# Kernel tuning notes

Hardware: AMD Instinct MI355X
Metric: run time of the kernel (lower is better)

Reference implementation:

```python
import jax, jax.numpy as jnp
import numpy as np
from jax import lax

B, T, C = 4, 1024, 1024
NH, HD = 16, 64
SCALE = 1.0 / np.sqrt(HD)
LN_EPS = 1e-5


def _layernorm(x, g, b):
    mu = jnp.mean(x, axis=-1, keepdims=True)
    var = jnp.var(x, axis=-1, keepdims=True)
    return (x - mu) * lax.rsqrt(var + LN_EPS) * g + b


def _compress(seg, w, g, b):
    # seg: [B, nH, L, hd]; depthwise Conv1d(k=2, s=2, p=1, groups=hd, no bias) + LayerNorm(hd)
    Bs, nH, L, hd = seg.shape
    xc = seg.reshape(Bs * nH, L, hd).transpose(0, 2, 1)  # [B*nH, hd, L]
    y = lax.conv_general_dilated(xc, w, window_strides=(2,), padding=[(1, 1)],
                                 dimension_numbers=('NCH', 'OIH', 'NCH'),
                                 feature_group_count=hd)  # [B*nH, hd, L//2+1]
    y = y.transpose(0, 2, 1)
    y = _layernorm(y, g, b)
    return y.reshape(Bs, nH, -1, hd)


def setup_inputs() -> dict:
    key = jax.random.key(0)
    ks = jax.random.split(key, 16)
    d = {
        'x': jax.random.normal(ks[0], (B, T, C), jnp.float32),
        'mem_k1': jax.random.normal(ks[1], (B, NH, 129, HD), jnp.float32),
        'mem_v1': jax.random.normal(ks[2], (B, NH, 129, HD), jnp.float32),
        'mem_k2': jax.random.normal(ks[3], (B, NH, 257, HD), jnp.float32),
        'mem_v2': jax.random.normal(ks[4], (B, NH, 257, HD), jnp.float32),
        'mem_k3': jax.random.normal(ks[5], (B, NH, 513, HD), jnp.float32),
        'mem_v3': jax.random.normal(ks[6], (B, NH, 513, HD), jnp.float32),
        'c_attn_w': jax.random.normal(ks[7], (3 * C, C), jnp.float32) * 0.02,
        'c_attn_b': jnp.zeros((3 * C,), jnp.float32),
        'c_proj_w': jax.random.normal(ks[8], (C, C), jnp.float32) * 0.02,
        'c_proj_b': jnp.zeros((C,), jnp.float32),
        'compress_k_w': jax.random.normal(ks[9], (HD, 1, 2), jnp.float32) * 0.5,
        'ln_k_g': jnp.ones((HD,), jnp.float32),
        'ln_k_b': jnp.zeros((HD,), jnp.float32),
        'compress_v_w': jax.random.normal(ks[10], (HD, 1, 2), jnp.float32) * 0.5,
        'ln_v_g': jnp.ones((HD,), jnp.float32),
        'ln_v_b': jnp.zeros((HD,), jnp.float32),
    }
    return d


def reference(x, mem_k1, mem_v1, mem_k2, mem_v2, mem_k3, mem_v3,
              c_attn_w, c_attn_b, c_proj_w, c_proj_b,
              compress_k_w, ln_k_g, ln_k_b, compress_v_w, ln_v_g, ln_v_b):
    # qkv projection
    qkv = x @ c_attn_w.T + c_attn_b  # [B, T, 3C]
    q, k_new, v_new = jnp.split(qkv, 3, axis=2)
    q = q.reshape(B, T, NH, HD).transpose(0, 2, 1, 3)       # [B, nH, T, hd]
    k_new = k_new.reshape(B, T, NH, HD).transpose(0, 2, 1, 3)
    v_new = v_new.reshape(B, T, NH, HD).transpose(0, 2, 1, 3)

    # compress the most recent cached segment (513 -> 257)
    k3c = _compress(mem_k3, compress_k_w, ln_k_g, ln_k_b)
    v3c = _compress(mem_v3, compress_v_w, ln_v_g, ln_v_b)

    all_k = jnp.concatenate([mem_k1, mem_k2, k3c, k_new], axis=2)  # [B, nH, T_mem, hd]
    all_v = jnp.concatenate([mem_v1, mem_v2, v3c, v_new], axis=2)
    T_mem = all_k.shape[2]

    att = jnp.einsum('bhqd,bhkd->bhqk', q, all_k) * SCALE  # [B, nH, T, T_mem]
    # causal mask taken from tril(block_size)[:T, :T_mem]: row i attends cols j <= i
    mask = jnp.arange(T)[:, None] >= jnp.arange(T_mem)[None, :]
    att = jnp.where(mask, att, -jnp.inf)
    att = jax.nn.softmax(att, axis=-1)
    y = jnp.einsum('bhqk,bhkd->bhqd', att, all_v)  # [B, nH, T, hd]
    y = y.transpose(0, 2, 1, 3).reshape(B, T, C)
    y = y @ c_proj_w.T + c_proj_b
    return y
```

## Files before the change

kernel.cpp:

```cpp
#include <hip/hip_runtime.h>


using u16    = unsigned short;
using bf16x8 = __attribute__((ext_vector_type(8))) __bf16;
using f32x4  = __attribute__((ext_vector_type(4))) float;
using u16x8  = __attribute__((ext_vector_type(8))) unsigned short;
using u16x4  = __attribute__((ext_vector_type(4))) unsigned short;

__device__ __forceinline__ u16 f2bf(float f) {
    union { float f; unsigned u; } v; v.f = f;
    unsigned r = v.u + 0x7FFFu + ((v.u >> 16) & 1u);
    return (u16)(r >> 16);
}

__device__ __forceinline__ void gload16(const void* src, const void* lds_base) {
    __builtin_amdgcn_global_load_lds(
        (const __attribute__((address_space(1))) void*)src,
        (__attribute__((address_space(3))) void*)lds_base, 16, 0, 0);
}

__global__ void cvt_f32_bf16(const float* __restrict__ src, u16* __restrict__ dst, int n4) {
    int i = blockIdx.x * blockDim.x + threadIdx.x;
    if (i >= n4) return;
    float4 f = reinterpret_cast<const float4*>(src)[i];
    u16x4 o; o[0] = f2bf(f.x); o[1] = f2bf(f.y); o[2] = f2bf(f.z); o[3] = f2bf(f.w);
    reinterpret_cast<u16x4*>(dst)[i] = o;
}

__global__ __launch_bounds__(64) void copy_mem_rows(const float* __restrict__ src,
                                                    u16* __restrict__ dst, int L, int ro) {
    int bh = blockIdx.y, t = blockIdx.x, d = threadIdx.x;
    float v = src[((size_t)bh * L + t) * 64 + d];
    dst[((size_t)bh * 1024 + ro + t) * 64 + d] = f2bf(v);
}

__global__ __launch_bounds__(64) void compress_ln(const float* __restrict__ src,
                                                  const float* __restrict__ w,
                                                  const float* __restrict__ g,
                                                  const float* __restrict__ bta,
                                                  u16* __restrict__ dst, int ro) {
    int bh = blockIdx.y, t = blockIdx.x, d = threadIdx.x;
    const float* seg = src + (size_t)bh * 513 * 64;
    float x0 = (t > 0) ? seg[(size_t)(2 * t - 1) * 64 + d] : 0.f;
    float x1 = seg[(size_t)(2 * t) * 64 + d];
    float y = w[2 * d] * x0 + w[2 * d + 1] * x1;
    float s = y;
    #pragma unroll
    for (int o = 32; o; o >>= 1) s += __shfl_xor(s, o);
    float mu = s * (1.f / 64.f);
    float dv = y - mu;
    float s2 = dv * dv;
    #pragma unroll
    for (int o = 32; o; o >>= 1) s2 += __shfl_xor(s2, o);
    float var = s2 * (1.f / 64.f);
    float out = dv * rsqrtf(var + 1e-5f) * g[d] + bta[d];
    dst[((size_t)bh * 1024 + ro + t) * 64 + d] = f2bf(out);
}

__global__ __launch_bounds__(256) void transpose_v(const u16* __restrict__ src,
                                                   u16* __restrict__ dst) {
    __shared__ u16 tile[64][66];
    const int bh = blockIdx.y, t0 = blockIdx.x * 64;
    const int tid = threadIdx.x;
    #pragma unroll
    for (int i = 0; i < 2; ++i) {
        int p = tid + i * 256;
        int tr = p >> 3, dc = (p & 7) * 8;
        *(u16x8*)&tile[tr][dc] = *(const u16x8*)&src[((size_t)bh * 1024 + t0 + tr) * 64 + dc];
    }
    __syncthreads();
    #pragma unroll
    for (int i = 0; i < 2; ++i) {
        int p = tid + i * 256;
        int d = p >> 3, tc = (p & 7) * 8;
        u16x8 v;
        #pragma unroll
        for (int e = 0; e < 8; ++e) v[e] = tile[tc + e][d];
        *(u16x8*)&dst[((size_t)bh * 64 + d) * 1024 + t0 + tc] = v;
    }
}

__global__ __launch_bounds__(256) void gemm128(const u16* __restrict__ A,
                                               const u16* __restrict__ Bw,
                                               const float* __restrict__ bias,
                                               int K, int N, int mode,
                                               float* __restrict__ outF,
                                               u16* __restrict__ q_buf,
                                               u16* __restrict__ all_k,
                                               u16* __restrict__ all_v) {
    __shared__ __align__(16) u16 Al[128 * 64];
    __shared__ __align__(16) u16 Bl[128 * 64];
    const int tid = threadIdx.x;
    const int wv = tid >> 6, lane = tid & 63;
    const int lg = lane >> 4, lr = lane & 15;
    const int wr = (wv >> 1) * 64, wc = (wv & 1) * 64;
    const int m0 = blockIdx.x * 128, n0 = blockIdx.y * 128;
    f32x4 acc[4][4] = {};
    const int ob0 = wv * 4096;
    for (int kt = 0; kt < K; kt += 64) {
        __syncthreads();
        #pragma unroll
        for (int c = 0; c < 4; ++c) {
            int ob = ob0 + c * 1024;
            int o = ob + lane * 16;
            int r = o >> 7, cb = o & 127;
            gload16((const char*)A + (((size_t)(m0 + r) * K + kt) << 1) + cb, (char*)Al + ob);
            gload16((const char*)Bw + (((size_t)(n0 + r) * K + kt) << 1) + cb, (char*)Bl + ob);
        }
        __syncthreads();
        #pragma unroll
        for (int dh = 0; dh < 2; ++dh) {
            bf16x8 af[4], bq[4];
            #pragma unroll
            for (int mi = 0; mi < 4; ++mi)
                af[mi] = *(const bf16x8*)&Al[(wr + mi * 16 + lr) * 64 + dh * 32 + lg * 8];
            #pragma unroll
            for (int ni = 0; ni < 4; ++ni)
                bq[ni] = *(const bf16x8*)&Bl[(wc + ni * 16 + lr) * 64 + dh * 32 + lg * 8];
            __builtin_amdgcn_s_setprio(1);
            #pragma unroll
            for (int mi = 0; mi < 4; ++mi)
                #pragma unroll
                for (int ni = 0; ni < 4; ++ni)
                    acc[mi][ni] = __builtin_amdgcn_mfma_f32_16x16x32_bf16(af[mi], bq[ni], acc[mi][ni], 0, 0, 0);
            __builtin_amdgcn_s_setprio(0);
        }
    }
    #pragma unroll
    for (int mi = 0; mi < 4; ++mi)
        #pragma unroll
        for (int ni = 0; ni < 4; ++ni)
            #pragma unroll
            for (int r = 0; r < 4; ++r) {
                int mm = m0 + wr + mi * 16 + lg * 4 + r;
                int nn = n0 + wc + ni * 16 + lr;
                float v = acc[mi][ni][r] + bias[nn];
                if (mode == 0) {
                    outF[(size_t)mm * N + nn] = v;
                } else {
                    int which = nn >> 10, c = nn & 1023, h = c >> 6, d = c & 63;
                    int b = mm >> 10, t = mm & 1023;
                    int bh = b * 16 + h;
                    if (which == 0) {
                        q_buf[((size_t)bh * 1024 + t) * 64 + d] = f2bf(v * 0.125f);
                    } else if (t < 381) {
                        u16* dst = (which == 1) ? all_k : all_v;
                        dst[((size_t)bh * 1024 + 643 + t) * 64 + d] = f2bf(v);
                    }
                }
            }
}

__global__ __launch_bounds__(256) void attn_kernel(const u16* __restrict__ Q,
                                                   const u16* __restrict__ Kc,
                                                   const u16* __restrict__ VT,
                                                   u16* __restrict__ Y) {
    __shared__ __align__(16) u16 Kl[2][4096];
    __shared__ __align__(16) u16 Vl[2][4096];
    __shared__ __align__(16) u16 P_w[4][16 * 64];
    const int tid = threadIdx.x;
    const int lane = tid & 63;
    const int w = tid >> 6;
    const int lg = lane >> 4, lr = lane & 15;
    const int bh = blockIdx.x;
    const int pair = blockIdx.y;
    const u16* Kb = Kc + (size_t)bh * 65536;
    const u16* Vb = VT + (size_t)bh * 65536;
    char* Pbase = (char*)&P_w[w][0];
    const int xorq = (lr & 7) << 4;

    const int r0 = tid >> 3,         c0 = ((tid & 7) * 16) ^ ((r0 & 7) << 4);
    const int r1 = (tid + 256) >> 3, c1 = ((tid & 7) * 16) ^ ((r1 & 7) << 4);
    const int dst0 = w * 1024;

    for (int phase = 0; phase < 2; ++phase) {
        const int qt = phase ? (15 - pair) : pair;
        const int q0 = qt * 64;
        const u16* Qb = Q + ((size_t)bh * 1024 + q0 + w * 16) * 64;
        bf16x8 qf0 = *(const bf16x8*)&Qb[lr * 64 + lg * 8];
        bf16x8 qf1 = *(const bf16x8*)&Qb[lr * 64 + 32 + lg * 8];
        f32x4 o[4] = {};
        float m = -1e30f, lsum = 0.f;
        const int i_q = q0 + w * 16 + lr;

        {
            const char* Ks = (const char*)Kb;
            gload16(Ks + ((size_t)r0 << 7) + c0, (char*)&Kl[0][0] + dst0);
            gload16(Ks + ((size_t)r1 << 7) + c1, (char*)&Kl[0][0] + 4096 + dst0);
            gload16((const char*)Vb + ((size_t)r0 << 11) + c0, (char*)&Vl[0][0] + dst0);
            gload16((const char*)Vb + ((size_t)r1 << 11) + c1, (char*)&Vl[0][0] + 4096 + dst0);
        }
        __syncthreads();
        int cur = 0;

        for (int kt = 0; kt <= qt; ++kt) {
            if (kt < qt) {
                const int k0n = (kt + 1) * 64;
                const char* Ks = (const char*)Kb + ((size_t)k0n << 7);
                const char* Vs = (const char*)Vb + ((size_t)k0n << 1);
                char* Kd = (char*)&Kl[cur ^ 1][0];
                char* Vd = (char*)&Vl[cur ^ 1][0];
                gload16(Ks + ((size_t)r0 << 7) + c0, Kd + dst0);
                gload16(Ks + ((size_t)r1 << 7) + c1, Kd + 4096 + dst0);
                gload16(Vs + ((size_t)r0 << 11) + c0, Vd + dst0);
                gload16(Vs + ((size_t)r1 << 11) + c1, Vd + 4096 + dst0);
            }
            const char* Kt = (const char*)&Kl[cur][0];
            const char* Vt = (const char*)&Vl[cur][0];
            f32x4 st[4] = {};
            __builtin_amdgcn_s_setprio(1);
            #pragma unroll
            for (int hh = 0; hh < 4; ++hh) {
                const char* Kr = Kt + (size_t)(hh * 16 + lr) * 128;
                bf16x8 kf0 = *(const bf16x8*)(Kr + ((lg * 16) ^ xorq));
                bf16x8 kf1 = *(const bf16x8*)(Kr + ((64 + lg * 16) ^ xorq));
                st[hh] = __builtin_amdgcn_mfma_f32_16x16x32_bf16(kf0, qf0, st[hh], 0, 0, 0);
                st[hh] = __builtin_amdgcn_mfma_f32_16x16x32_bf16(kf1, qf1, st[hh], 0, 0, 0);
            }
            __builtin_amdgcn_s_setprio(0);
            const int k0 = kt * 64;
            float sv[16];
            float tmax = -1e30f;
            if (kt == qt) {
                #pragma unroll
                for (int hh = 0; hh < 4; ++hh)
                    #pragma unroll
                    for (int r = 0; r < 4; ++r) {
                        int j = k0 + hh * 16 + lg * 4 + r;
                        float s = (j <= i_q) ? st[hh][r] : -1e30f;
                        sv[hh * 4 + r] = s;
                        tmax = fmaxf(tmax, s);
                    }
            } else {
                #pragma unroll
                for (int hh = 0; hh < 4; ++hh)
                    #pragma unroll
                    for (int r = 0; r < 4; ++r) {
                        float s = st[hh][r];
                        sv[hh * 4 + r] = s;
                        tmax = fmaxf(tmax, s);
                    }
            }
            tmax = fmaxf(tmax, __shfl_xor(tmax, 16));
            tmax = fmaxf(tmax, __shfl_xor(tmax, 32));
            if (!__all(tmax - m <= 8.f)) {
                float mnew = fmaxf(m, tmax);
                float alpha = __expf(m - mnew);
                #pragma unroll
                for (int c = 0; c < 4; ++c) {
                    o[c][0] *= alpha; o[c][1] *= alpha; o[c][2] *= alpha; o[c][3] *= alpha;
                }
                lsum *= alpha;
                m = mnew;
            }
            float psum = 0.f;
            #pragma unroll
            for (int hh = 0; hh < 4; ++hh) {
                u16x4 pk;
                #pragma unroll
                for (int r = 0; r < 4; ++r) {
                    float p = __expf(sv[hh * 4 + r] - m);
                    psum += p;
                    pk[r] = f2bf(p);
                }
                *(u16x4*)(Pbase + lr * 128 + ((hh * 32 + lg * 8) ^ xorq)) = pk;
            }
            psum += __shfl_xor(psum, 16);
            psum += __shfl_xor(psum, 32);
            lsum += psum;
            asm volatile("s_waitcnt lgkmcnt(0)" ::: "memory");
            __builtin_amdgcn_sched_barrier(0);
            #pragma unroll
            for (int ks = 0; ks < 2; ++ks) {
                bf16x8 pf = *(const bf16x8*)(Pbase + lr * 128 + ((ks * 64 + lg * 16) ^ xorq));
                __builtin_amdgcn_s_setprio(1);
                #pragma unroll
                for (int c = 0; c < 4; ++c) {
                    const char* Vr = Vt + (size_t)(c * 16 + lr) * 128;
                    bf16x8 vf = *(const bf16x8*)(Vr + ((ks * 64 + lg * 16) ^ xorq));
                    o[c] = __builtin_amdgcn_mfma_f32_16x16x32_bf16(vf, pf, o[c], 0, 0, 0);
                }
                __builtin_amdgcn_s_setprio(0);
            }
            __syncthreads();
            cur ^= 1;
        }
        float inv = 1.0f / lsum;
        #pragma unroll
        for (int c = 0; c < 4; ++c) {
            u16x4 ov;
            #pragma unroll
            for (int r = 0; r < 4; ++r) ov[r] = f2bf(o[c][r] * inv);
            *(u16x4*)(Pbase + lr * 128 + (((c * 16 + lg * 4) * 2) ^ xorq)) = ov;
        }
        asm volatile("s_waitcnt lgkmcnt(0)" ::: "memory");
        __builtin_amdgcn_sched_barrier(0);
        const int b = bh >> 4, h = bh & 15;
        const int qr = lane >> 2, dseg = (lane & 3) * 16;
        const int xorr = (qr & 7) << 4;
        size_t g = ((size_t)(b * 1024 + q0 + w * 16 + qr)) * 1024 + h * 64 + dseg;
        *(u16x8*)&Y[g]     = *(const u16x8*)(Pbase + qr * 128 + ((dseg * 2) ^ xorr));
        *(u16x8*)&Y[g + 8] = *(const u16x8*)(Pbase + qr * 128 + ((dseg * 2 + 16) ^ xorr));
    }
}

extern "C" void kernel_launch(void* const* d_in, const int* in_sizes, int n_in,
                              void* d_out, int out_size, void* d_ws, size_t ws_size,
                              hipStream_t stream) {
    const float* x            = (const float*)d_in[0];
    const float* mem_k1       = (const float*)d_in[1];
    const float* mem_v1       = (const float*)d_in[2];
    const float* mem_k2       = (const float*)d_in[3];
    const float* mem_v2       = (const float*)d_in[4];
    const float* mem_k3       = (const float*)d_in[5];
    const float* mem_v3       = (const float*)d_in[6];
    const float* c_attn_w     = (const float*)d_in[7];
    const float* c_attn_b     = (const float*)d_in[8];
    const float* c_proj_w     = (const float*)d_in[9];
    const float* c_proj_b     = (const float*)d_in[10];
    const float* compress_k_w = (const float*)d_in[11];
    const float* ln_k_g       = (const float*)d_in[12];
    const float* ln_k_b       = (const float*)d_in[13];
    const float* compress_v_w = (const float*)d_in[14];
    const float* ln_v_g       = (const float*)d_in[15];
    const float* ln_v_b       = (const float*)d_in[16];

    char* ws = (char*)d_ws;
    u16* x_bf   = (u16*)(ws);
    u16* all_vT = (u16*)(ws);
    u16* wq_bf  = (u16*)(ws + (8u << 20));
    u16* wp_bf  = (u16*)(ws + (14u << 20));
    u16* q_buf  = (u16*)(ws + (16u << 20));
    u16* all_k  = (u16*)(ws + (24u << 20));
    u16* all_v  = (u16*)(ws + (32u << 20));
    u16* att_y  = (u16*)(ws + (40u << 20));
    float* out = (float*)d_out;

    cvt_f32_bf16<<<4096, 256, 0, stream>>>(x, x_bf, 1048576);
    cvt_f32_bf16<<<3072, 256, 0, stream>>>(c_attn_w, wq_bf, 786432);
    cvt_f32_bf16<<<1024, 256, 0, stream>>>(c_proj_w, wp_bf, 262144);

    copy_mem_rows<<<dim3(129, 64), 64, 0, stream>>>(mem_k1, all_k, 129, 0);
    copy_mem_rows<<<dim3(129, 64), 64, 0, stream>>>(mem_v1, all_v, 129, 0);
    copy_mem_rows<<<dim3(257, 64), 64, 0, stream>>>(mem_k2, all_k, 257, 129);
    copy_mem_rows<<<dim3(257, 64), 64, 0, stream>>>(mem_v2, all_v, 257, 129);

    compress_ln<<<dim3(257, 64), 64, 0, stream>>>(mem_k3, compress_k_w, ln_k_g, ln_k_b, all_k, 386);
    compress_ln<<<dim3(257, 64), 64, 0, stream>>>(mem_v3, compress_v_w, ln_v_g, ln_v_b, all_v, 386);

    gemm128<<<dim3(32, 24), 256, 0, stream>>>(x_bf, wq_bf, c_attn_b, 1024, 3072, 1,
                                              nullptr, q_buf, all_k, all_v);

    transpose_v<<<dim3(16, 64), 256, 0, stream>>>(all_v, all_vT);

    attn_kernel<<<dim3(64, 8), 256, 0, stream>>>(q_buf, all_k, all_vT, att_y);

    gemm128<<<dim3(32, 8), 256, 0, stream>>>(att_y, wp_bf, c_proj_b, 1024, 1024, 0,
                                             out, nullptr, nullptr, nullptr);
}
```

Before: 140.4 us.

## Double-buffer GEMM LDS tiles and XOR-swizzle to avoid bank conflicts

Converts the bf16 GEMM main loop to a double-buffered LDS scheme that issues the next K-tile's global-to-LDS loads before computing on the current tile, with one barrier per iteration. It also applies an XOR swizzle on the column offset of each loaded row so fragment reads from LDS spread across banks. This doubles LDS usage to 64KB per block, which may lower occupancy, and relies on the barrier waiting for the async LDS loads.

```diff
diff --git a/kernel.cpp b/kernel.cpp
--- a/kernel.cpp
+++ b/kernel.cpp
@@ -88,8 +88,8 @@
                                                u16* __restrict__ q_buf,
                                                u16* __restrict__ all_k,
                                                u16* __restrict__ all_v) {
-    __shared__ __align__(16) u16 Al[128 * 64];
-    __shared__ __align__(16) u16 Bl[128 * 64];
+    __shared__ __align__(16) u16 Al[2][128 * 64];
+    __shared__ __align__(16) u16 Bl[2][128 * 64];
     const int tid = threadIdx.x;
     const int wv = tid >> 6, lane = tid & 63;
     const int lg = lane >> 4, lr = lane & 15;
@@ -97,26 +97,50 @@
     const int m0 = blockIdx.x * 128, n0 = blockIdx.y * 128;
     f32x4 acc[4][4] = {};
     const int ob0 = wv * 4096;
-    for (int kt = 0; kt < K; kt += 64) {
-        __syncthreads();
-        #pragma unroll
-        for (int c = 0; c < 4; ++c) {
-            int ob = ob0 + c * 1024;
-            int o = ob + lane * 16;
-            int r = o >> 7, cb = o & 127;
-            gload16((const char*)A + (((size_t)(m0 + r) * K + kt) << 1) + cb, (char*)Al + ob);
-            gload16((const char*)Bw + (((size_t)(n0 + r) * K + kt) << 1) + cb, (char*)Bl + ob);
-        }
-        __syncthreads();
+    int srow[4], scol[4];
+    #pragma unroll
+    for (int c = 0; c < 4; ++c) {
+        int o = ob0 + c * 1024 + lane * 16;
+        int r = o >> 7;
+        srow[c] = r;
+        scol[c] = (o & 127) ^ ((r & 7) << 4);
+    }
+    const int nk = K >> 6;
+    #pragma unroll
+    for (int c = 0; c < 4; ++c) {
+        int ob = ob0 + c * 1024;
+        gload16((const char*)A  + (((size_t)(m0 + srow[c]) * K) << 1) + scol[c], (char*)&Al[0][0] + ob);
+        gload16((const char*)Bw + (((size_t)(n0 + srow[c]) * K) << 1) + scol[c], (char*)&Bl[0][0] + ob);
+    }
+    __syncthreads();
+    int cur = 0;
+    for (int kt = 0; kt < nk; ++kt) {
+        if (kt + 1 < nk) {
+            const size_t ko = (size_t)(kt + 1) << 6;
+            #pragma unroll
+            for (int c = 0; c < 4; ++c) {
+                int ob = ob0 + c * 1024;
+                gload16((const char*)A  + (((size_t)(m0 + srow[c]) * K + ko) << 1) + scol[c],
+                        (char*)&Al[cur ^ 1][0] + ob);
+                gload16((const char*)Bw + (((size_t)(n0 + srow[c]) * K + ko) << 1) + scol[c],
+                        (char*)&Bl[cur ^ 1][0] + ob);
+            }
+        }
+        const char* At = (const char*)&Al[cur][0];
+        const char* Bt = (const char*)&Bl[cur][0];
         #pragma unroll
         for (int dh = 0; dh < 2; ++dh) {
             bf16x8 af[4], bq[4];
             #pragma unroll
-            for (int mi = 0; mi < 4; ++mi)
-                af[mi] = *(const bf16x8*)&Al[(wr + mi * 16 + lr) * 64 + dh * 32 + lg * 8];
-            #pragma unroll
-            for (int ni = 0; ni < 4; ++ni)
-                bq[ni] = *(const bf16x8*)&Bl[(wc + ni * 16 + lr) * 64 + dh * 32 + lg * 8];
+            for (int mi = 0; mi < 4; ++mi) {
+                int row = wr + mi * 16 + lr;
+                af[mi] = *(const bf16x8*)(At + row * 128 + ((dh * 64 + lg * 16) ^ ((row & 7) << 4)));
+            }
+            #pragma unroll
+            for (int ni = 0; ni < 4; ++ni) {
+                int row = wc + ni * 16 + lr;
+                bq[ni] = *(const bf16x8*)(Bt + row * 128 + ((dh * 64 + lg * 16) ^ ((row & 7) << 4)));
+            }
             __builtin_amdgcn_s_setprio(1);
             #pragma unroll
             for (int mi = 0; mi < 4; ++mi)
@@ -125,6 +149,8 @@
                     acc[mi][ni] = __builtin_amdgcn_mfma_f32_16x16x32_bf16(af[mi], bq[ni], acc[mi][ni], 0, 0, 0);
             __builtin_amdgcn_s_setprio(0);
         }
+        __syncthreads();
+        cur ^= 1;
     }
     #pragma unroll
     for (int mi = 0; mi < 4; ++mi)
```

Measured after the change: 145.8 us. 3.9% more time.

## Double-buffer GEMM LDS tiles with XOR swizzle and XCD-aware block remap

Applied to the files above, without the earlier changes.

Restructures the bf16 GEMM main loop to use two 128x32 LDS buffers per operand, issuing the next K-slice's global-to-LDS loads before the current slice's MFMAs so memory latency overlaps compute. It also applies an XOR swizzle to the LDS column layout to reduce bank conflicts, and remaps block IDs so consecutive tiles spread across the 8 XCDs. The K step halves to 32, which doubles the number of barriers and loop iterations. The remap assumes the grid size is divisible by 8.

```diff
diff --git a/kernel.cpp b/kernel.cpp
--- a/kernel.cpp
+++ b/kernel.cpp
@@ -88,43 +88,60 @@
                                                u16* __restrict__ q_buf,
                                                u16* __restrict__ all_k,
                                                u16* __restrict__ all_v) {
-    __shared__ __align__(16) u16 Al[128 * 64];
-    __shared__ __align__(16) u16 Bl[128 * 64];
+    __shared__ __align__(16) u16 Al[2][128 * 32];
+    __shared__ __align__(16) u16 Bl[2][128 * 32];
     const int tid = threadIdx.x;
     const int wv = tid >> 6, lane = tid & 63;
     const int lg = lane >> 4, lr = lane & 15;
     const int wr = (wv >> 1) * 64, wc = (wv & 1) * 64;
-    const int m0 = blockIdx.x * 128, n0 = blockIdx.y * 128;
+    const int id = blockIdx.x + blockIdx.y * gridDim.x;
+    const int per = (gridDim.x * gridDim.y) >> 3;
+    const int nid = (id & 7) * per + (id >> 3);
+    const int m0 = (nid % gridDim.x) * 128, n0 = (nid / gridDim.x) * 128;
     f32x4 acc[4][4] = {};
-    const int ob0 = wv * 4096;
-    for (int kt = 0; kt < K; kt += 64) {
+    const int sr0 = tid >> 2,         sc0 = (((tid & 3) << 4)) ^ (((sr0 >> 1) & 3) << 4);
+    const int sr1 = (tid + 256) >> 2, sc1 = (((tid & 3) << 4)) ^ (((sr1 >> 1) & 3) << 4);
+    const int dA0 = wv * 1024;
+    const int dA1 = 4096 + wv * 1024;
+    const int nk = K >> 5;
+    gload16((const char*)A  + (((size_t)(m0 + sr0) * K) << 1) + sc0, (char*)&Al[0][0] + dA0);
+    gload16((const char*)A  + (((size_t)(m0 + sr1) * K) << 1) + sc1, (char*)&Al[0][0] + dA1);
+    gload16((const char*)Bw + (((size_t)(n0 + sr0) * K) << 1) + sc0, (char*)&Bl[0][0] + dA0);
+    gload16((const char*)Bw + (((size_t)(n0 + sr1) * K) << 1) + sc1, (char*)&Bl[0][0] + dA1);
+    __syncthreads();
+    int cur = 0;
+    for (int kt = 0; kt < nk; ++kt) {
+        const char* At = (const char*)&Al[cur][0];
+        const char* Bt = (const char*)&Bl[cur][0];
+        bf16x8 af[4], bq[4];
+        #pragma unroll
+        for (int mi = 0; mi < 4; ++mi) {
+            int row = wr + mi * 16 + lr;
+            af[mi] = *(const bf16x8*)(At + row * 64 + ((lg << 4) ^ (((row >> 1) & 3) << 4)));
+        }
+        #pragma unroll
+        for (int ni = 0; ni < 4; ++ni) {
+            int row = wc + ni * 16 + lr;
+            bq[ni] = *(const bf16x8*)(Bt + row * 64 + ((lg << 4) ^ (((row >> 1) & 3) << 4)));
+        }
+        if (kt + 1 < nk) {
+            const size_t ko = (size_t)(kt + 1) << 5;
+            char* Ad = (char*)&Al[cur ^ 1][0];
+            char* Bd = (char*)&Bl[cur ^ 1][0];
+            gload16((const char*)A  + (((size_t)(m0 + sr0) * K + ko) << 1) + sc0, Ad + dA0);
+            gload16((const char*)A  + (((size_t)(m0 + sr1) * K + ko) << 1) + sc1, Ad + dA1);
+            gload16((const char*)Bw + (((size_t)(n0 + sr0) * K + ko) << 1) + sc0, Bd + dA0);
+            gload16((const char*)Bw + (((size_t)(n0 + sr1) * K + ko) << 1) + sc1, Bd + dA1);
+        }
+        __builtin_amdgcn_s_setprio(1);
+        #pragma unroll
+        for (int mi = 0; mi < 4; ++mi)
+            #pragma unroll
+            for (int ni = 0; ni < 4; ++ni)
+                acc[mi][ni] = __builtin_amdgcn_mfma_f32_16x16x32_bf16(af[mi], bq[ni], acc[mi][ni], 0, 0, 0);
+        __builtin_amdgcn_s_setprio(0);
         __syncthreads();
-        #pragma unroll
-        for (int c = 0; c < 4; ++c) {
-            int ob = ob0 + c * 1024;
-            int o = ob + lane * 16;
-            int r = o >> 7, cb = o & 127;
-            gload16((const char*)A + (((size_t)(m0 + r) * K + kt) << 1) + cb, (char*)Al + ob);
-            gload16((const char*)Bw + (((size_t)(n0 + r) * K + kt) << 1) + cb, (char*)Bl + ob);
-        }
-        __syncthreads();
-        #pragma unroll
-        for (int dh = 0; dh < 2; ++dh) {
-            bf16x8 af[4], bq[4];
-            #pragma unroll
-            for (int mi = 0; mi < 4; ++mi)
-                af[mi] = *(const bf16x8*)&Al[(wr + mi * 16 + lr) * 64 + dh * 32 + lg * 8];
-            #pragma unroll
-            for (int ni = 0; ni < 4; ++ni)
-                bq[ni] = *(const bf16x8*)&Bl[(wc + ni * 16 + lr) * 64 + dh * 32 + lg * 8];
-            __builtin_amdgcn_s_setprio(1);
-            #pragma unroll
-            for (int mi = 0; mi < 4; ++mi)
-                #pragma unroll
-                for (int ni = 0; ni < 4; ++ni)
-                    acc[mi][ni] = __builtin_amdgcn_mfma_f32_16x16x32_bf16(af[mi], bq[ni], acc[mi][ni], 0, 0, 0);
-            __builtin_amdgcn_s_setprio(0);
-        }
+        cur ^= 1;
     }
     #pragma unroll
     for (int mi = 0; mi < 4; ++mi)
```

Result: faster. 133.0 us (-5.3%).

## Replace 128x128 GEMM with 256x256 triple-buffered swizzled pipelined GEMM

Applied to the files above, without the earlier changes.

Swaps the 128x128 bf16 MFMA GEMM for a 256x256-tile kernel with 512 threads. It triple-buffers LDS, loading 32-wide K slices through global_load_lds, and overlaps the next stages' loads with MFMA work using explicit waitcnt, barriers and scheduling hints. It also adds an XOR swizzle on LDS rows to avoid bank conflicts and an XCD-aware block-to-tile remap for L2 locality. The larger tiles raise data reuse per block but cut the grid to 192 and 64 blocks, which may leave many CUs idle on both projections.

```diff
diff --git a/kernel.cpp b/kernel.cpp
--- a/kernel.cpp
+++ b/kernel.cpp
@@ -80,54 +80,102 @@
     }
 }
 
-__global__ __launch_bounds__(256) void gemm128(const u16* __restrict__ A,
-                                               const u16* __restrict__ Bw,
-                                               const float* __restrict__ bias,
-                                               int K, int N, int mode,
-                                               float* __restrict__ outF,
-                                               u16* __restrict__ q_buf,
-                                               u16* __restrict__ all_k,
-                                               u16* __restrict__ all_v) {
-    __shared__ __align__(16) u16 Al[128 * 64];
-    __shared__ __align__(16) u16 Bl[128 * 64];
-    const int tid = threadIdx.x;
-    const int wv = tid >> 6, lane = tid & 63;
+__global__ __launch_bounds__(512, 2) void gemm256p(const u16* __restrict__ A,
+                                                   const u16* __restrict__ Bw,
+                                                   const float* __restrict__ bias,
+                                                   int K, int N, int mode,
+                                                   float* __restrict__ outF,
+                                                   u16* __restrict__ q_buf,
+                                                   u16* __restrict__ all_k,
+                                                   u16* __restrict__ all_v) {
+    __shared__ __align__(16) u16 S[3][4][4096];
+    const int t = threadIdx.x;
+    const int wv = t >> 6, lane = t & 63;
     const int lg = lane >> 4, lr = lane & 15;
-    const int wr = (wv >> 1) * 64, wc = (wv & 1) * 64;
-    const int m0 = blockIdx.x * 128, n0 = blockIdx.y * 128;
-    f32x4 acc[4][4] = {};
-    const int ob0 = wv * 4096;
-    for (int kt = 0; kt < K; kt += 64) {
-        __syncthreads();
-        #pragma unroll
-        for (int c = 0; c < 4; ++c) {
-            int ob = ob0 + c * 1024;
-            int o = ob + lane * 16;
-            int r = o >> 7, cb = o & 127;
-            gload16((const char*)A + (((size_t)(m0 + r) * K + kt) << 1) + cb, (char*)Al + ob);
-            gload16((const char*)Bw + (((size_t)(n0 + r) * K + kt) << 1) + cb, (char*)Bl + ob);
-        }
-        __syncthreads();
-        #pragma unroll
-        for (int dh = 0; dh < 2; ++dh) {
-            bf16x8 af[4], bq[4];
-            #pragma unroll
-            for (int mi = 0; mi < 4; ++mi)
-                af[mi] = *(const bf16x8*)&Al[(wr + mi * 16 + lr) * 64 + dh * 32 + lg * 8];
+    const int wr = (wv >> 2) * 128, wc = (wv & 3) * 64;
+    const int rhalf = wv >> 2;
+    const int chalf = (wv & 3) >> 1;
+    const int cbase = (wv & 1) * 64;
+    const int id = blockIdx.x + blockIdx.y * gridDim.x;
+    const int pm = gridDim.x >> 2, pn = gridDim.y >> 1;
+    const int xcd = id & 7, lid = id >> 3;
+    const int m0 = ((xcd >> 1) * pm + lid % pm) * 256;
+    const int n0 = ((xcd & 1) * pn + lid / pm) * 256;
+    f32x4 acc[8][4] = {};
+    const int srow = t >> 2;
+    const int scol = ((t & 3) << 4) ^ (((srow >> 1) & 3) << 4);
+    const int sdst = wv * 1024;
+    const int nt = K >> 5;
+
+    auto stageA = [&](int T) {
+        char* base = (char*)&S[T % 3][0][0];
+        const size_t ko = (size_t)T << 5;
+        gload16((const char*)A + (((size_t)(m0 + srow) * K + ko) << 1) + scol, base + sdst);
+        gload16((const char*)A + (((size_t)(m0 + 128 + srow) * K + ko) << 1) + scol,
+                base + 8192 + sdst);
+    };
+    auto stageB = [&](int T) {
+        char* base = (char*)&S[T % 3][2][0];
+        const size_t ko = (size_t)T << 5;
+        gload16((const char*)Bw + (((size_t)(n0 + srow) * K + ko) << 1) + scol, base + sdst);
+        gload16((const char*)Bw + (((size_t)(n0 + 128 + srow) * K + ko) << 1) + scol,
+                base + 8192 + sdst);
+    };
+    stageA(0); stageB(0); stageA(1); stageB(1);
+    asm volatile("s_waitcnt vmcnt(4)" ::: "memory");
+    __builtin_amdgcn_s_barrier();
+    __builtin_amdgcn_sched_barrier(0);
+
+    for (int T = 0; T < nt; ++T) {
+        const char* Ah = (const char*)&S[T % 3][rhalf][0];
+        const char* Bh = (const char*)&S[T % 3][2 + chalf][0];
+        bf16x8 af[4], bq[4];
+        #pragma unroll
+        for (int mi = 0; mi < 4; ++mi) {
+            int rr = mi * 16 + lr;
+            af[mi] = *(const bf16x8*)(Ah + rr * 64 + ((lg << 4) ^ (((rr >> 1) & 3) << 4)));
+        }
+        #pragma unroll
+        for (int ni = 0; ni < 4; ++ni) {
+            int rr = cbase + ni * 16 + lr;
+            bq[ni] = *(const bf16x8*)(Bh + rr * 64 + ((lg << 4) ^ (((rr >> 1) & 3) << 4)));
+        }
+        if (T + 2 < nt) stageA(T + 2);
+        __builtin_amdgcn_s_barrier();
+        asm volatile("s_waitcnt lgkmcnt(0)" ::: "memory");
+        __builtin_amdgcn_sched_barrier(0);
+        __builtin_amdgcn_s_setprio(1);
+        #pragma unroll
+        for (int mi = 0; mi < 4; ++mi)
             #pragma unroll
             for (int ni = 0; ni < 4; ++ni)
-                bq[ni] = *(const bf16x8*)&Bl[(wc + ni * 16 + lr) * 64 + dh * 32 + lg * 8];
-            __builtin_amdgcn_s_setprio(1);
-            #pragma unroll
-            for (int mi = 0; mi < 4; ++mi)
-                #pragma unroll
-                for (int ni = 0; ni < 4; ++ni)
-                    acc[mi][ni] = __builtin_amdgcn_mfma_f32_16x16x32_bf16(af[mi], bq[ni], acc[mi][ni], 0, 0, 0);
-            __builtin_amdgcn_s_setprio(0);
+                acc[mi][ni] = __builtin_amdgcn_mfma_f32_16x16x32_bf16(af[mi], bq[ni], acc[mi][ni], 0, 0, 0);
+        __builtin_amdgcn_s_setprio(0);
+        __builtin_amdgcn_s_barrier();
+        #pragma unroll
+        for (int mi = 0; mi < 4; ++mi) {
+            int rr = (mi + 4) * 16 + lr;
+            af[mi] = *(const bf16x8*)(Ah + rr * 64 + ((lg << 4) ^ (((rr >> 1) & 3) << 4)));
+        }
+        if (T + 2 < nt) stageB(T + 2);
+        asm volatile("s_waitcnt lgkmcnt(0)" ::: "memory");
+        __builtin_amdgcn_sched_barrier(0);
+        __builtin_amdgcn_s_setprio(1);
+        #pragma unroll
+        for (int mi = 0; mi < 4; ++mi)
+            #pragma unroll
+            for (int ni = 0; ni < 4; ++ni)
+                acc[mi + 4][ni] = __builtin_amdgcn_mfma_f32_16x16x32_bf16(af[mi], bq[ni], acc[mi + 4][ni], 0, 0, 0);
+        __builtin_amdgcn_s_setprio(0);
+        if (T + 1 < nt) {
+            if (T + 2 < nt) asm volatile("s_waitcnt vmcnt(4)" ::: "memory");
+            else            asm volatile("s_waitcnt vmcnt(0)" ::: "memory");
+            __builtin_amdgcn_s_barrier();
+            __builtin_amdgcn_sched_barrier(0);
         }
     }
     #pragma unroll
-    for (int mi = 0; mi < 4; ++mi)
+    for (int mi = 0; mi < 8; ++mi)
         #pragma unroll
         for (int ni = 0; ni < 4; ++ni)
             #pragma unroll
@@ -139,13 +187,13 @@
                     outF[(size_t)mm * N + nn] = v;
                 } else {
                     int which = nn >> 10, c = nn & 1023, h = c >> 6, d = c & 63;
-                    int b = mm >> 10, t = mm & 1023;
+                    int b = mm >> 10, tt = mm & 1023;
                     int bh = b * 16 + h;
                     if (which == 0) {
-                        q_buf[((size_t)bh * 1024 + t) * 64 + d] = f2bf(v * 0.125f);
-                    } else if (t < 381) {
+                        q_buf[((size_t)bh * 1024 + tt) * 64 + d] = f2bf(v * 0.125f);
+                    } else if (tt < 381) {
                         u16* dst = (which == 1) ? all_k : all_v;
-                        dst[((size_t)bh * 1024 + 643 + t) * 64 + d] = f2bf(v);
+                        dst[((size_t)bh * 1024 + 643 + tt) * 64 + d] = f2bf(v);
                     }
                 }
             }
@@ -348,13 +396,13 @@
     compress_ln<<<dim3(257, 64), 64, 0, stream>>>(mem_k3, compress_k_w, ln_k_g, ln_k_b, all_k, 386);
     compress_ln<<<dim3(257, 64), 64, 0, stream>>>(mem_v3, compress_v_w, ln_v_g, ln_v_b, all_v, 386);
 
-    gemm128<<<dim3(32, 24), 256, 0, stream>>>(x_bf, wq_bf, c_attn_b, 1024, 3072, 1,
-                                              nullptr, q_buf, all_k, all_v);
+    gemm256p<<<dim3(16, 12), 512, 0, stream>>>(x_bf, wq_bf, c_attn_b, 1024, 3072, 1,
+                                               nullptr, q_buf, all_k, all_v);
 
     transpose_v<<<dim3(16, 64), 256, 0, stream>>>(all_v, all_vT);
 
     attn_kernel<<<dim3(64, 8), 256, 0, stream>>>(q_buf, all_k, all_vT, att_y);
 
-    gemm128<<<dim3(32, 8), 256, 0, stream>>>(att_y, wp_bf, c_proj_b, 1024, 1024, 0,
-                                             out, nullptr, nullptr, nullptr);
-}
+    gemm256p<<<dim3(16, 4), 512, 0, stream>>>(att_y, wp_bf, c_proj_b, 1024, 1024, 0,
+                                              out, nullptr, nullptr, nullptr);
+}
```

New measurement: 156.6 us. 1.12x slower.
